# Performance work log

Hardware: AMD Instinct MI355X
Metric: run time of the kernel (lower is better)

Reference implementation:

```python
import jax, jax.numpy as jnp
import numpy as np

NUM_USER = 200000
NUM_ITEM = 100000
DIM = 64
NUM_LAYER = 2  # hardcoded in LightGCN.__init__ (lgn_single(..., num_layer=2))
AVG_DEG = 16
N = NUM_USER + NUM_ITEM
E = N * AVG_DEG
BATCH = 16384


def setup_inputs() -> dict:
    key = jax.random.key(0)
    k = jax.random.split(key, 8)
    emb_user = jax.random.normal(k[0], (NUM_USER, DIM), jnp.float32) * 0.05
    emb_item = jax.random.normal(k[1], (NUM_ITEM, DIM), jnp.float32) * 0.05
    # COO sparse normalized adjacency: out[row] += vals * x[col]
    graph_row = jax.random.randint(k[2], (E,), 0, N, dtype=jnp.int32)
    graph_col = jax.random.randint(k[3], (E,), 0, N, dtype=jnp.int32)
    graph_vals = jax.random.uniform(k[4], (E,), jnp.float32) / AVG_DEG
    user_nodes = jax.random.randint(k[5], (BATCH,), 0, NUM_USER, dtype=jnp.int32)
    pos_item_nodes = jax.random.randint(k[6], (BATCH,), 0, NUM_ITEM, dtype=jnp.int32) + NUM_USER
    neg_item_nodes = jax.random.randint(k[7], (BATCH,), 0, NUM_ITEM, dtype=jnp.int32) + NUM_USER
    return {
        "emb_user": emb_user,
        "emb_item": emb_item,
        "graph_vals": graph_vals,
        "graph_row": graph_row,
        "graph_col": graph_col,
        "user_nodes": user_nodes,
        "pos_item_nodes": pos_item_nodes,
        "neg_item_nodes": neg_item_nodes,
    }


def _spmm(vals, row, col, x):
    # torch.sparse.mm(graph, x) with graph in COO form
    return jax.ops.segment_sum(vals[:, None] * x[col], row, num_segments=N)


def reference(emb_user, emb_item, graph_vals, graph_row, graph_col,
              user_nodes, pos_item_nodes, neg_item_nodes):
    # LGN_single.forward: concat, propagate, mean over layer stack
    all_emb = jnp.concatenate([emb_user, emb_item], axis=0)  # [N, D]
    acc = all_emb
    e = all_emb
    for _ in range(NUM_LAYER):
        e = _spmm(graph_vals, graph_row, graph_col, e)
        acc = acc + e
    light_out = acc / (NUM_LAYER + 1)  # mean of stacked embeddings
    # LightGCN.forward: gather + elementwise dot scores
    u = light_out[user_nodes]          # [B, D]
    p = light_out[pos_item_nodes]      # [B, D]
    n = light_out[neg_item_nodes]      # [B, D]
    pos_scores = jnp.sum(u * p, axis=1)
    neg_scores = jnp.sum(u * n, axis=1)
    return jnp.stack([pos_scores, neg_scores])  # [2, B]
```

## Files before the change

### kernel.cpp

```cpp
#include <hip/hip_runtime.h>

#define DIM 64
#define CHUNK 8192
#define MAXNB 512
#define BSHIFT 10
#define RPB 1024
#define PADMASK 7

__device__ __forceinline__ unsigned short f2bf(float f) {
    unsigned int u = __float_as_uint(f);
    return (unsigned short)((u + 0x7FFFu + ((u >> 16) & 1u)) >> 16);
}
__device__ __forceinline__ float4 bf2f4(uint2 g) {
    float4 x;
    x.x = __uint_as_float(g.x << 16);
    x.y = __uint_as_float(g.x & 0xffff0000u);
    x.z = __uint_as_float(g.y << 16);
    x.w = __uint_as_float(g.y & 0xffff0000u);
    return x;
}

__device__ __forceinline__ int blockScan256(int v, int* sh) {
    int t = threadIdx.x;
    sh[t] = v;
    __syncthreads();
    for (int off = 1; off < 256; off <<= 1) {
        int x = (t >= off) ? sh[t - off] : 0;
        __syncthreads();
        sh[t] += x;
        __syncthreads();
    }
    return sh[t];
}


__global__ void conv2_k(const float* __restrict__ u, const float* __restrict__ it,
                        int nu, int ntot, unsigned short* __restrict__ o) {
    int i = blockIdx.x * blockDim.x + threadIdx.x;
    int stride = gridDim.x * blockDim.x;
    int n8 = ntot >> 3;
    for (int t = i; t < n8; t += stride) {
        int e = t * 8;
        const float* src = (e < nu) ? (u + e) : (it + (e - nu));
        float4 x = *(const float4*)src;
        float4 y = *(const float4*)(src + 4);
        uint4 v;
        v.x = (unsigned)f2bf(x.x) | ((unsigned)f2bf(x.y) << 16);
        v.y = (unsigned)f2bf(x.z) | ((unsigned)f2bf(x.w) << 16);
        v.z = (unsigned)f2bf(y.x) | ((unsigned)f2bf(y.y) << 16);
        v.w = (unsigned)f2bf(y.z) | ((unsigned)f2bf(y.w) << 16);
        ((uint4*)o)[t] = v;
    }
}


__global__ void p1a_hist(const int* __restrict__ row, int E, int NB,
                         int* __restrict__ counts) {
    __shared__ int h[MAXNB];
    for (int b = threadIdx.x; b < NB; b += 256) h[b] = 0;
    __syncthreads();
    int base = blockIdx.x * CHUNK;
    int end = min(base + CHUNK, E);
    int vend = base + ((end - base) & ~3);
    for (int i = base + threadIdx.x * 4; i < vend; i += 1024) {
        int4 r = *(const int4*)(row + i);
        atomicAdd(&h[r.x >> BSHIFT], 1);
        atomicAdd(&h[r.y >> BSHIFT], 1);
        atomicAdd(&h[r.z >> BSHIFT], 1);
        atomicAdd(&h[r.w >> BSHIFT], 1);
    }
    for (int i = vend + threadIdx.x; i < end; i += 256) atomicAdd(&h[row[i] >> BSHIFT], 1);
    __syncthreads();
    int blk = blockIdx.x;
    for (int b = threadIdx.x; b < NB; b += 256) counts[(size_t)blk * NB + b] = h[b];
}

__global__ void p1b_scan(int* __restrict__ counts, int NBLK, int NB,
                         int* __restrict__ bucketTotal) {
    int b = blockIdx.x, t = threadIdx.x;
    __shared__ int sh[256];
    int v[8];
    int run = 0;
#pragma unroll
    for (int i = 0; i < 8; i++) {
        int idx = t * 8 + i;
        int c = (idx < NBLK) ? counts[(size_t)idx * NB + b] : 0;
        v[i] = run;
        run += c;
    }
    int inc = blockScan256(run, sh);
    int excl = inc - run;
#pragma unroll
    for (int i = 0; i < 8; i++) {
        int idx = t * 8 + i;
        if (idx < NBLK) counts[(size_t)idx * NB + b] = v[i] + excl;
    }
    if (t == 255) bucketTotal[b] = sh[255];
}

__global__ void p_scan_tot(const int* __restrict__ bucketTotal, int NB,
                           int* __restrict__ bucketStart) {
    int t = threadIdx.x;
    __shared__ int sh[256];
    int v[8];
    int run = 0;
#pragma unroll
    for (int i = 0; i < 8; i++) {
        int idx = t * 8 + i;
        int c = (idx < NB) ? bucketTotal[idx] : 0;
        v[i] = run;
        run += c;
    }
    int inc = blockScan256(run, sh);
    int excl = inc - run;
#pragma unroll
    for (int i = 0; i < 8; i++) {
        int idx = t * 8 + i;
        if (idx < NB) bucketStart[idx] = v[i] + excl;
    }
    if (t == 255) bucketStart[NB] = sh[255];
}

__global__ void p1c_scatter(const int* __restrict__ row, const int* __restrict__ col,
                            const float* __restrict__ vals, int E, int NB,
                            const int* __restrict__ counts, const int* __restrict__ bucketStart,
                            int2* __restrict__ bdata) {
    __shared__ int cur[MAXNB];
    int blk = blockIdx.x;
    for (int b = threadIdx.x; b < NB; b += 256)
        cur[b] = bucketStart[b] + counts[(size_t)blk * NB + b];
    __syncthreads();
    int base = blk * CHUNK;
    int end = min(base + CHUNK, E);
    int vend = base + ((end - base) & ~3);
    for (int i = base + threadIdx.x * 4; i < vend; i += 1024) {
        int4 r = *(const int4*)(row + i);
        int4 c = *(const int4*)(col + i);
        float4 v = *(const float4*)(vals + i);
        int p0 = atomicAdd(&cur[r.x >> BSHIFT], 1);
        int p1 = atomicAdd(&cur[r.y >> BSHIFT], 1);
        int p2 = atomicAdd(&cur[r.z >> BSHIFT], 1);
        int p3 = atomicAdd(&cur[r.w >> BSHIFT], 1);
        bdata[p0] = make_int2(((r.x & (RPB - 1)) << 20) | c.x, __float_as_int(v.x));
        bdata[p1] = make_int2(((r.y & (RPB - 1)) << 20) | c.y, __float_as_int(v.y));
        bdata[p2] = make_int2(((r.z & (RPB - 1)) << 20) | c.z, __float_as_int(v.z));
        bdata[p3] = make_int2(((r.w & (RPB - 1)) << 20) | c.w, __float_as_int(v.w));
    }
    for (int i = vend + threadIdx.x; i < end; i += 256) {
        int r = row[i];
        int p = atomicAdd(&cur[r >> BSHIFT], 1);
        bdata[p] = make_int2(((r & (RPB - 1)) << 20) | col[i], __float_as_int(vals[i]));
    }
}

__global__ void p2_group(const int2* __restrict__ bdata, const int* __restrict__ bucketStart,
                         int NB, int N, int padSlop,
                         int* __restrict__ rowStart, int* __restrict__ rowLen,
                         int2* __restrict__ pairs) {
    __shared__ int hist[RPB];
    __shared__ int sh[256];
    __shared__ int cur[RPB];
    int b = blockIdx.x, t = threadIdx.x;
    int s0 = bucketStart[b], s1 = bucketStart[b + 1];
    int pbase = s0 + b * padSlop;
    for (int i = t; i < RPB; i += 256) hist[i] = 0;
    __syncthreads();
    for (int i = s0 + t; i < s1; i += 256)
        atomicAdd(&hist[(bdata[i].x >> 20) & (RPB - 1)], 1);
    __syncthreads();
    int v[4];
    int run = 0;
#pragma unroll
    for (int i = 0; i < 4; i++) {
        int h = hist[t * 4 + i];
        int hp = (h + PADMASK) & ~PADMASK;
        v[i] = run;
        run += hp;
    }
    int inc = blockScan256(run, sh);
    int excl = inc - run;
#pragma unroll
    for (int i = 0; i < 4; i++) {
        int r = (b << BSHIFT) + t * 4 + i;
        int st = excl + v[i];
        if (r < N) {
            int h = hist[t * 4 + i];
            rowStart[r] = pbase + st;
            rowLen[r] = (h + PADMASK) & ~PADMASK;
        }
        cur[t * 4 + i] = st;
    }
    __syncthreads();
    for (int i = s0 + t; i < s1; i += 256) {
        int2 e = bdata[i];
        int rl = (e.x >> 20) & (RPB - 1);
        int pos = atomicAdd(&cur[rl], 1);
        pairs[pbase + pos] = make_int2((e.x & 0xFFFFF) << 7, e.y);
    }
    __syncthreads();
#pragma unroll
    for (int i = 0; i < 4; i++) {
        int h = hist[t * 4 + i];
        int hp = (h + PADMASK) & ~PADMASK;
        int st = excl + v[i];
        for (int p = st + h; p < st + hp; p++)
            pairs[pbase + p] = make_int2(0, 0);
    }
}


__global__ void spmm1_k(const unsigned short* __restrict__ emb16,
                        const int* __restrict__ rowStart, const int* __restrict__ rowLen,
                        const int2* __restrict__ pairs,
                        int n_total, unsigned short* __restrict__ e1) {
    int wave = (blockIdx.x * blockDim.x + threadIdx.x) >> 6;
    int lane = threadIdx.x & 63;
    if (wave >= n_total) return;
    int eg = lane >> 4, dp = lane & 15;
    unsigned off0 = dp * 8u;
    const char* base = (const char*)emb16;
    int len = rowLen[wave];
    const int2* pp = pairs + rowStart[wave];
    float4 a0 = {0.f, 0.f, 0.f, 0.f}, a1 = {0.f, 0.f, 0.f, 0.f};
    float4 a2 = {0.f, 0.f, 0.f, 0.f}, a3 = {0.f, 0.f, 0.f, 0.f};
    int k = 0;
    for (; k + 16 <= len; k += 16) {
        int4 q0 = *(const int4*)(pp + k + 2 * eg);
        int4 q1 = *(const int4*)(pp + k + 8 + 2 * eg);
        uint2 g0 = *(const uint2*)(base + ((unsigned)q0.x + off0));
        uint2 g1 = *(const uint2*)(base + ((unsigned)q0.z + off0));
        uint2 g2 = *(const uint2*)(base + ((unsigned)q1.x + off0));
        uint2 g3 = *(const uint2*)(base + ((unsigned)q1.z + off0));
        float v0 = __int_as_float(q0.y), v1 = __int_as_float(q0.w);
        float v2 = __int_as_float(q1.y), v3 = __int_as_float(q1.w);
        float4 x0 = bf2f4(g0), x1 = bf2f4(g1), x2 = bf2f4(g2), x3 = bf2f4(g3);
        a0.x += v0 * x0.x; a0.y += v0 * x0.y; a0.z += v0 * x0.z; a0.w += v0 * x0.w;
        a1.x += v1 * x1.x; a1.y += v1 * x1.y; a1.z += v1 * x1.z; a1.w += v1 * x1.w;
        a2.x += v2 * x2.x; a2.y += v2 * x2.y; a2.z += v2 * x2.z; a2.w += v2 * x2.w;
        a3.x += v3 * x3.x; a3.y += v3 * x3.y; a3.z += v3 * x3.z; a3.w += v3 * x3.w;
    }
    for (; k < len; k += 8) {
        int4 q0 = *(const int4*)(pp + k + 2 * eg);
        uint2 g0 = *(const uint2*)(base + ((unsigned)q0.x + off0));
        uint2 g1 = *(const uint2*)(base + ((unsigned)q0.z + off0));
        float v0 = __int_as_float(q0.y), v1 = __int_as_float(q0.w);
        float4 x0 = bf2f4(g0), x1 = bf2f4(g1);
        a0.x += v0 * x0.x; a0.y += v0 * x0.y; a0.z += v0 * x0.z; a0.w += v0 * x0.w;
        a1.x += v1 * x1.x; a1.y += v1 * x1.y; a1.z += v1 * x1.z; a1.w += v1 * x1.w;
    }
    float4 s;
    s.x = (a0.x + a1.x) + (a2.x + a3.x);
    s.y = (a0.y + a1.y) + (a2.y + a3.y);
    s.z = (a0.z + a1.z) + (a2.z + a3.z);
    s.w = (a0.w + a1.w) + (a2.w + a3.w);
    s.x += __shfl_xor(s.x, 16); s.y += __shfl_xor(s.y, 16);
    s.z += __shfl_xor(s.z, 16); s.w += __shfl_xor(s.w, 16);
    s.x += __shfl_xor(s.x, 32); s.y += __shfl_xor(s.y, 32);
    s.z += __shfl_xor(s.z, 32); s.w += __shfl_xor(s.w, 32);
    if (eg == 0) {
        uint2 o;
        o.x = (unsigned)f2bf(s.x) | ((unsigned)f2bf(s.y) << 16);
        o.y = (unsigned)f2bf(s.z) | ((unsigned)f2bf(s.w) << 16);
        *(uint2*)(e1 + (size_t)wave * DIM + dp * 4) = o;
    }
}


__global__ void final_k(const float* __restrict__ emb_user, const float* __restrict__ emb_item,
                        int n_user, const unsigned short* __restrict__ e1,
                        const int* __restrict__ rowStart, const int* __restrict__ rowLen,
                        const int2* __restrict__ pairs,
                        const int* __restrict__ u_nodes, const int* __restrict__ p_nodes,
                        const int* __restrict__ n_nodes, int B, float* __restrict__ out) {
    int wave = (blockIdx.x * blockDim.x + threadIdx.x) >> 6;
    int lane = threadIdx.x & 63;
    if (wave >= B) return;
    int eg = lane >> 4, dp = lane & 15;
    unsigned off0 = dp * 8u;
    const char* base = (const char*)e1;
    int nid[3] = {u_nodes[wave], p_nodes[wave], n_nodes[wave]};
    float4 l[3];
#pragma unroll
    for (int j = 0; j < 3; j++) {
        int r = nid[j];
        const float* base0 = (r < n_user) ? (emb_user + (size_t)r * DIM)
                                          : (emb_item + (size_t)(r - n_user) * DIM);
        float4 acc = *(const float4*)(base0 + dp * 4);
        float4 t1 = bf2f4(*(const uint2*)(e1 + (size_t)r * DIM + dp * 4));
        acc.x += t1.x; acc.y += t1.y; acc.z += t1.z; acc.w += t1.w;
        int len = rowLen[r];
        const int2* pp = pairs + rowStart[r];
        float4 a0 = {0.f, 0.f, 0.f, 0.f}, a1 = {0.f, 0.f, 0.f, 0.f};
        float4 a2 = {0.f, 0.f, 0.f, 0.f}, a3 = {0.f, 0.f, 0.f, 0.f};
        int k = 0;
        for (; k + 16 <= len; k += 16) {
            int4 q0 = *(const int4*)(pp + k + 2 * eg);
            int4 q1 = *(const int4*)(pp + k + 8 + 2 * eg);
            uint2 g0 = *(const uint2*)(base + ((unsigned)q0.x + off0));
            uint2 g1 = *(const uint2*)(base + ((unsigned)q0.z + off0));
            uint2 g2 = *(const uint2*)(base + ((unsigned)q1.x + off0));
            uint2 g3 = *(const uint2*)(base + ((unsigned)q1.z + off0));
            float v0 = __int_as_float(q0.y), v1 = __int_as_float(q0.w);
            float v2 = __int_as_float(q1.y), v3 = __int_as_float(q1.w);
            float4 x0 = bf2f4(g0), x1 = bf2f4(g1), x2 = bf2f4(g2), x3 = bf2f4(g3);
            a0.x += v0 * x0.x; a0.y += v0 * x0.y; a0.z += v0 * x0.z; a0.w += v0 * x0.w;
            a1.x += v1 * x1.x; a1.y += v1 * x1.y; a1.z += v1 * x1.z; a1.w += v1 * x1.w;
            a2.x += v2 * x2.x; a2.y += v2 * x2.y; a2.z += v2 * x2.z; a2.w += v2 * x2.w;
            a3.x += v3 * x3.x; a3.y += v3 * x3.y; a3.z += v3 * x3.z; a3.w += v3 * x3.w;
        }
        for (; k < len; k += 8) {
            int4 q0 = *(const int4*)(pp + k + 2 * eg);
            uint2 g0 = *(const uint2*)(base + ((unsigned)q0.x + off0));
            uint2 g1 = *(const uint2*)(base + ((unsigned)q0.z + off0));
            float v0 = __int_as_float(q0.y), v1 = __int_as_float(q0.w);
            float4 x0 = bf2f4(g0), x1 = bf2f4(g1);
            a0.x += v0 * x0.x; a0.y += v0 * x0.y; a0.z += v0 * x0.z; a0.w += v0 * x0.w;
            a1.x += v1 * x1.x; a1.y += v1 * x1.y; a1.z += v1 * x1.z; a1.w += v1 * x1.w;
        }
        float4 s;
        s.x = (a0.x + a1.x) + (a2.x + a3.x);
        s.y = (a0.y + a1.y) + (a2.y + a3.y);
        s.z = (a0.z + a1.z) + (a2.z + a3.z);
        s.w = (a0.w + a1.w) + (a2.w + a3.w);
        s.x += __shfl_xor(s.x, 16); s.y += __shfl_xor(s.y, 16);
        s.z += __shfl_xor(s.z, 16); s.w += __shfl_xor(s.w, 16);
        s.x += __shfl_xor(s.x, 32); s.y += __shfl_xor(s.y, 32);
        s.z += __shfl_xor(s.z, 32); s.w += __shfl_xor(s.w, 32);
        l[j].x = (acc.x + s.x) * (1.0f / 3.0f);
        l[j].y = (acc.y + s.y) * (1.0f / 3.0f);
        l[j].z = (acc.z + s.z) * (1.0f / 3.0f);
        l[j].w = (acc.w + s.w) * (1.0f / 3.0f);
    }
    float ps = l[0].x * l[1].x + l[0].y * l[1].y + l[0].z * l[1].z + l[0].w * l[1].w;
    float ns = l[0].x * l[2].x + l[0].y * l[2].y + l[0].z * l[2].z + l[0].w * l[2].w;
    ps += __shfl_xor(ps, 1); ns += __shfl_xor(ns, 1);
    ps += __shfl_xor(ps, 2); ns += __shfl_xor(ns, 2);
    ps += __shfl_xor(ps, 4); ns += __shfl_xor(ns, 4);
    ps += __shfl_xor(ps, 8); ns += __shfl_xor(ns, 8);
    if (lane == 0) {
        out[wave] = ps;
        out[B + wave] = ns;
    }
}

extern "C" void kernel_launch(void* const* d_in, const int* in_sizes, int n_in,
                              void* d_out, int out_size, void* d_ws, size_t ws_size,
                              hipStream_t stream) {
    const float* emb_user = (const float*)d_in[0];
    const float* emb_item = (const float*)d_in[1];
    const float* gvals    = (const float*)d_in[2];
    const int*   grow     = (const int*)d_in[3];
    const int*   gcol     = (const int*)d_in[4];
    const int*   unodes   = (const int*)d_in[5];
    const int*   pnodes   = (const int*)d_in[6];
    const int*   nnodes   = (const int*)d_in[7];
    float* out = (float*)d_out;

    int n_user = in_sizes[0] / DIM;
    int n_item = in_sizes[1] / DIM;
    int N = n_user + n_item;
    int E = in_sizes[2];
    int B = in_sizes[5];
    int NB = (N + RPB - 1) >> BSHIFT;
    int NBLK = (E + CHUNK - 1) / CHUNK;
    int padSlop = RPB * PADMASK;

    char* ws = (char*)d_ws;
    size_t off = 0;
    auto alloc = [&](size_t bytes) -> void* {
        void* p = ws + off;
        off = (off + bytes + 255) & ~(size_t)255;
        return p;
    };
    size_t embBytes = (size_t)N * DIM * 2;
    size_t countsBytes = (size_t)NBLK * NB * 4;
    size_t regionBBytes = (size_t)E * 8 > embBytes ? (size_t)E * 8 : embBytes;
    size_t regionABytes = countsBytes > embBytes ? countsBytes : embBytes;
    size_t pairsBytes = ((size_t)E + (size_t)NB * padSlop) * 8;

    int*  rowStart    = (int*)alloc((size_t)N * 4);
    int*  rowLen      = (int*)alloc((size_t)N * 4);
    int*  bucketTotal = (int*)alloc((size_t)MAXNB * 4);
    int*  bucketStart = (int*)alloc((size_t)(MAXNB + 1) * 4);
    int2* pairs       = (int2*)alloc(pairsBytes);
    char* regionB = (char*)alloc(regionBBytes);
    int2*           bdata = (int2*)regionB;
    unsigned short* emb16 = (unsigned short*)regionB;
    char* regionA = (char*)alloc(regionABytes);
    int*            counts = (int*)regionA;
    unsigned short* e1     = (unsigned short*)regionA;
    (void)n_in; (void)out_size; (void)ws_size;

    p1a_hist<<<NBLK, 256, 0, stream>>>(grow, E, NB, counts);
    p1b_scan<<<NB, 256, 0, stream>>>(counts, NBLK, NB, bucketTotal);
    p_scan_tot<<<1, 256, 0, stream>>>(bucketTotal, NB, bucketStart);
    p1c_scatter<<<NBLK, 256, 0, stream>>>(grow, gcol, gvals, E, NB, counts, bucketStart, bdata);
    p2_group<<<NB, 256, 0, stream>>>(bdata, bucketStart, NB, N, padSlop,
                                     rowStart, rowLen, pairs);

    conv2_k<<<2048, 256, 0, stream>>>(emb_user, emb_item, n_user * DIM, N * DIM, emb16);

    spmm1_k<<<(N + 3) / 4, 256, 0, stream>>>(emb16, rowStart, rowLen, pairs, N, e1);
    final_k<<<(B + 3) / 4, 256, 0, stream>>>(emb_user, emb_item, n_user, e1,
                                             rowStart, rowLen, pairs,
                                             unodes, pnodes, nnodes, B, out);
}
```

Before: 307.4 us.

## Fuse bf16 embedding conversion into histogram kernel and use nontemporal streaming loads

When the workspace is large enough, the bf16 embedding buffer gets its own region instead of aliasing the COO bucket buffer. The float-to-bf16 conversion can then run as extra blocks inside the histogram kernel rather than as a separate launch after grouping. Streaming reads of row/col/vals, bdata, rowStart/rowLen and the pairs array become nontemporal loads, so they are less likely to evict the embedding rows that are gathered from cache. The cost is extra workspace and a runtime branch on workspace size, with the old aliasing path kept as a fallback.

```diff
diff --git a/kernel.cpp b/kernel.cpp
--- a/kernel.cpp
+++ b/kernel.cpp
@@ -6,6 +6,12 @@
 #define BSHIFT 10
 #define RPB 1024
 #define PADMASK 7
+#define CONVB 1024
+
+typedef int   iv2 __attribute__((ext_vector_type(2)));
+typedef int   iv4 __attribute__((ext_vector_type(4)));
+typedef float fv4 __attribute__((ext_vector_type(4)));
+#define NTL(p) __builtin_nontemporal_load(p)
 
 __device__ __forceinline__ unsigned short f2bf(float f) {
     unsigned int u = __float_as_uint(f);
@@ -34,45 +40,45 @@
 }
 
 
-__global__ void conv2_k(const float* __restrict__ u, const float* __restrict__ it,
-                        int nu, int ntot, unsigned short* __restrict__ o) {
-    int i = blockIdx.x * blockDim.x + threadIdx.x;
-    int stride = gridDim.x * blockDim.x;
-    int n8 = ntot >> 3;
-    for (int t = i; t < n8; t += stride) {
-        int e = t * 8;
-        const float* src = (e < nu) ? (u + e) : (it + (e - nu));
-        float4 x = *(const float4*)src;
-        float4 y = *(const float4*)(src + 4);
-        uint4 v;
-        v.x = (unsigned)f2bf(x.x) | ((unsigned)f2bf(x.y) << 16);
-        v.y = (unsigned)f2bf(x.z) | ((unsigned)f2bf(x.w) << 16);
-        v.z = (unsigned)f2bf(y.x) | ((unsigned)f2bf(y.y) << 16);
-        v.w = (unsigned)f2bf(y.z) | ((unsigned)f2bf(y.w) << 16);
-        ((uint4*)o)[t] = v;
-    }
-}
-
-
-__global__ void p1a_hist(const int* __restrict__ row, int E, int NB,
-                         int* __restrict__ counts) {
+__global__ void p1a_conv(const int* __restrict__ row, int E, int NB,
+                         int* __restrict__ counts,
+                         const float* __restrict__ u, const float* __restrict__ it,
+                         int nu, int ntot, unsigned short* __restrict__ o, int NBLK) {
     __shared__ int h[MAXNB];
-    for (int b = threadIdx.x; b < NB; b += 256) h[b] = 0;
-    __syncthreads();
-    int base = blockIdx.x * CHUNK;
-    int end = min(base + CHUNK, E);
-    int vend = base + ((end - base) & ~3);
-    for (int i = base + threadIdx.x * 4; i < vend; i += 1024) {
-        int4 r = *(const int4*)(row + i);
-        atomicAdd(&h[r.x >> BSHIFT], 1);
-        atomicAdd(&h[r.y >> BSHIFT], 1);
-        atomicAdd(&h[r.z >> BSHIFT], 1);
-        atomicAdd(&h[r.w >> BSHIFT], 1);
-    }
-    for (int i = vend + threadIdx.x; i < end; i += 256) atomicAdd(&h[row[i] >> BSHIFT], 1);
-    __syncthreads();
     int blk = blockIdx.x;
-    for (int b = threadIdx.x; b < NB; b += 256) counts[(size_t)blk * NB + b] = h[b];
+    if (blk < NBLK) {
+        for (int b = threadIdx.x; b < NB; b += 256) h[b] = 0;
+        __syncthreads();
+        int base = blk * CHUNK;
+        int end = min(base + CHUNK, E);
+        int vend = base + ((end - base) & ~3);
+        for (int i = base + threadIdx.x * 4; i < vend; i += 1024) {
+            iv4 r = NTL((const iv4*)(row + i));
+            atomicAdd(&h[r.x >> BSHIFT], 1);
+            atomicAdd(&h[r.y >> BSHIFT], 1);
+            atomicAdd(&h[r.z >> BSHIFT], 1);
+            atomicAdd(&h[r.w >> BSHIFT], 1);
+        }
+        for (int i = vend + threadIdx.x; i < end; i += 256) atomicAdd(&h[row[i] >> BSHIFT], 1);
+        __syncthreads();
+        for (int b = threadIdx.x; b < NB; b += 256) counts[(size_t)blk * NB + b] = h[b];
+    } else {
+        int i = (blk - NBLK) * 256 + threadIdx.x;
+        int stride = CONVB * 256;
+        int n8 = ntot >> 3;
+        for (int t = i; t < n8; t += stride) {
+            int e = t * 8;
+            const float* src = (e < nu) ? (u + e) : (it + (e - nu));
+            fv4 x = NTL((const fv4*)src);
+            fv4 y = NTL((const fv4*)(src + 4));
+            uint4 v;
+            v.x = (unsigned)f2bf(x.x) | ((unsigned)f2bf(x.y) << 16);
+            v.y = (unsigned)f2bf(x.z) | ((unsigned)f2bf(x.w) << 16);
+            v.z = (unsigned)f2bf(y.x) | ((unsigned)f2bf(y.y) << 16);
+            v.w = (unsigned)f2bf(y.z) | ((unsigned)f2bf(y.w) << 16);
+            ((uint4*)o)[t] = v;
+        }
+    }
 }
 
 __global__ void p1b_scan(int* __restrict__ counts, int NBLK, int NB,
@@ -134,9 +140,9 @@
     int end = min(base + CHUNK, E);
     int vend = base + ((end - base) & ~3);
     for (int i = base + threadIdx.x * 4; i < vend; i += 1024) {
-        int4 r = *(const int4*)(row + i);
-        int4 c = *(const int4*)(col + i);
-        float4 v = *(const float4*)(vals + i);
+        iv4 r = NTL((const iv4*)(row + i));
+        iv4 c = NTL((const iv4*)(col + i));
+        fv4 v = NTL((const fv4*)(vals + i));
         int p0 = atomicAdd(&cur[r.x >> BSHIFT], 1);
         int p1 = atomicAdd(&cur[r.y >> BSHIFT], 1);
         int p2 = atomicAdd(&cur[r.z >> BSHIFT], 1);
@@ -192,7 +198,7 @@
     }
     __syncthreads();
     for (int i = s0 + t; i < s1; i += 256) {
-        int2 e = bdata[i];
+        iv2 e = NTL((const iv2*)(bdata + i));
         int rl = (e.x >> 20) & (RPB - 1);
         int pos = atomicAdd(&cur[rl], 1);
         pairs[pbase + pos] = make_int2((e.x & 0xFFFFF) << 7, e.y);
@@ -219,14 +225,14 @@
     int eg = lane >> 4, dp = lane & 15;
     unsigned off0 = dp * 8u;
     const char* base = (const char*)emb16;
-    int len = rowLen[wave];
-    const int2* pp = pairs + rowStart[wave];
+    int len = NTL(rowLen + wave);
+    const int2* pp = pairs + NTL(rowStart + wave);
     float4 a0 = {0.f, 0.f, 0.f, 0.f}, a1 = {0.f, 0.f, 0.f, 0.f};
     float4 a2 = {0.f, 0.f, 0.f, 0.f}, a3 = {0.f, 0.f, 0.f, 0.f};
     int k = 0;
     for (; k + 16 <= len; k += 16) {
-        int4 q0 = *(const int4*)(pp + k + 2 * eg);
-        int4 q1 = *(const int4*)(pp + k + 8 + 2 * eg);
+        iv4 q0 = NTL((const iv4*)(pp + k + 2 * eg));
+        iv4 q1 = NTL((const iv4*)(pp + k + 8 + 2 * eg));
         uint2 g0 = *(const uint2*)(base + ((unsigned)q0.x + off0));
         uint2 g1 = *(const uint2*)(base + ((unsigned)q0.z + off0));
         uint2 g2 = *(const uint2*)(base + ((unsigned)q1.x + off0));
@@ -240,7 +246,7 @@
         a3.x += v3 * x3.x; a3.y += v3 * x3.y; a3.z += v3 * x3.z; a3.w += v3 * x3.w;
     }
     for (; k < len; k += 8) {
-        int4 q0 = *(const int4*)(pp + k + 2 * eg);
+        iv4 q0 = NTL((const iv4*)(pp + k + 2 * eg));
         uint2 g0 = *(const uint2*)(base + ((unsigned)q0.x + off0));
         uint2 g1 = *(const uint2*)(base + ((unsigned)q0.z + off0));
         float v0 = __int_as_float(q0.y), v1 = __int_as_float(q0.w);
@@ -294,8 +300,8 @@
         float4 a2 = {0.f, 0.f, 0.f, 0.f}, a3 = {0.f, 0.f, 0.f, 0.f};
         int k = 0;
         for (; k + 16 <= len; k += 16) {
-            int4 q0 = *(const int4*)(pp + k + 2 * eg);
-            int4 q1 = *(const int4*)(pp + k + 8 + 2 * eg);
+            iv4 q0 = NTL((const iv4*)(pp + k + 2 * eg));
+            iv4 q1 = NTL((const iv4*)(pp + k + 8 + 2 * eg));
             uint2 g0 = *(const uint2*)(base + ((unsigned)q0.x + off0));
             uint2 g1 = *(const uint2*)(base + ((unsigned)q0.z + off0));
             uint2 g2 = *(const uint2*)(base + ((unsigned)q1.x + off0));
@@ -309,7 +315,7 @@
             a3.x += v3 * x3.x; a3.y += v3 * x3.y; a3.z += v3 * x3.z; a3.w += v3 * x3.w;
         }
         for (; k < len; k += 8) {
-            int4 q0 = *(const int4*)(pp + k + 2 * eg);
+            iv4 q0 = NTL((const iv4*)(pp + k + 2 * eg));
             uint2 g0 = *(const uint2*)(base + ((unsigned)q0.x + off0));
             uint2 g1 = *(const uint2*)(base + ((unsigned)q0.z + off0));
             float v0 = __int_as_float(q0.y), v1 = __int_as_float(q0.w);
@@ -343,6 +349,25 @@
     }
 }
 
+__global__ void conv2_k(const float* __restrict__ u, const float* __restrict__ it,
+                        int nu, int ntot, unsigned short* __restrict__ o) {
+    int i = blockIdx.x * blockDim.x + threadIdx.x;
+    int stride = gridDim.x * blockDim.x;
+    int n8 = ntot >> 3;
+    for (int t = i; t < n8; t += stride) {
+        int e = t * 8;
+        const float* src = (e < nu) ? (u + e) : (it + (e - nu));
+        fv4 x = NTL((const fv4*)src);
+        fv4 y = NTL((const fv4*)(src + 4));
+        uint4 v;
+        v.x = (unsigned)f2bf(x.x) | ((unsigned)f2bf(x.y) << 16);
+        v.y = (unsigned)f2bf(x.z) | ((unsigned)f2bf(x.w) << 16);
+        v.z = (unsigned)f2bf(y.x) | ((unsigned)f2bf(y.y) << 16);
+        v.w = (unsigned)f2bf(y.z) | ((unsigned)f2bf(y.w) << 16);
+        ((uint4*)o)[t] = v;
+    }
+}
+
 extern "C" void kernel_launch(void* const* d_in, const int* in_sizes, int n_in,
                               void* d_out, int out_size, void* d_ws, size_t ws_size,
                               hipStream_t stream) {
@@ -365,6 +390,17 @@
     int NBLK = (E + CHUNK - 1) / CHUNK;
     int padSlop = RPB * PADMASK;
 
+    auto align256 = [](size_t x) { return (x + 255) & ~(size_t)255; };
+    size_t embBytes = (size_t)N * DIM * 2;
+    size_t countsBytes = (size_t)NBLK * NB * 4;
+    size_t bdataBytes = (size_t)E * 8;
+    size_t regionABytes = countsBytes > embBytes ? countsBytes : embBytes;
+    size_t pairsBytes = ((size_t)E + (size_t)NB * padSlop) * 8;
+    size_t fixedBytes = align256((size_t)N * 4) * 2 + align256((size_t)MAXNB * 4) +
+                        align256((size_t)(MAXNB + 1) * 4) + align256(pairsBytes) +
+                        align256(regionABytes);
+    bool sepEmb = fixedBytes + align256(bdataBytes) + align256(embBytes) <= ws_size;
+
     char* ws = (char*)d_ws;
     size_t off = 0;
     auto alloc = [&](size_t bytes) -> void* {
@@ -372,33 +408,37 @@
         off = (off + bytes + 255) & ~(size_t)255;
         return p;
     };
-    size_t embBytes = (size_t)N * DIM * 2;
-    size_t countsBytes = (size_t)NBLK * NB * 4;
-    size_t regionBBytes = (size_t)E * 8 > embBytes ? (size_t)E * 8 : embBytes;
-    size_t regionABytes = countsBytes > embBytes ? countsBytes : embBytes;
-    size_t pairsBytes = ((size_t)E + (size_t)NB * padSlop) * 8;
-
     int*  rowStart    = (int*)alloc((size_t)N * 4);
     int*  rowLen      = (int*)alloc((size_t)N * 4);
     int*  bucketTotal = (int*)alloc((size_t)MAXNB * 4);
     int*  bucketStart = (int*)alloc((size_t)(MAXNB + 1) * 4);
     int2* pairs       = (int2*)alloc(pairsBytes);
-    char* regionB = (char*)alloc(regionBBytes);
-    int2*           bdata = (int2*)regionB;
-    unsigned short* emb16 = (unsigned short*)regionB;
+    int2* bdata;
+    unsigned short* emb16;
+    if (sepEmb) {
+        bdata = (int2*)alloc(bdataBytes);
+        emb16 = (unsigned short*)alloc(embBytes);
+    } else {
+        char* regionB = (char*)alloc(bdataBytes > embBytes ? bdataBytes : embBytes);
+        bdata = (int2*)regionB;
+        emb16 = (unsigned short*)regionB;
+    }
     char* regionA = (char*)alloc(regionABytes);
     int*            counts = (int*)regionA;
     unsigned short* e1     = (unsigned short*)regionA;
-    (void)n_in; (void)out_size; (void)ws_size;
-
-    p1a_hist<<<NBLK, 256, 0, stream>>>(grow, E, NB, counts);
+    (void)n_in; (void)out_size;
+
+    int nConv = sepEmb ? CONVB : 0;
+    p1a_conv<<<NBLK + nConv, 256, 0, stream>>>(grow, E, NB, counts,
+                                               emb_user, emb_item, n_user * DIM, N * DIM,
+                                               emb16, NBLK);
     p1b_scan<<<NB, 256, 0, stream>>>(counts, NBLK, NB, bucketTotal);
     p_scan_tot<<<1, 256, 0, stream>>>(bucketTotal, NB, bucketStart);
     p1c_scatter<<<NBLK, 256, 0, stream>>>(grow, gcol, gvals, E, NB, counts, bucketStart, bdata);
     p2_group<<<NB, 256, 0, stream>>>(bdata, bucketStart, NB, N, padSlop,
                                      rowStart, rowLen, pairs);
-
-    conv2_k<<<2048, 256, 0, stream>>>(emb_user, emb_item, n_user * DIM, N * DIM, emb16);
+    if (!sepEmb)
+        conv2_k<<<2048, 256, 0, stream>>>(emb_user, emb_item, n_user * DIM, N * DIM, emb16);
 
     spmm1_k<<<(N + 3) / 4, 256, 0, stream>>>(emb16, rowStart, rowLen, pairs, N, e1);
     final_k<<<(B + 3) / 4, 256, 0, stream>>>(emb_user, emb_item, n_user, e1,
```

Result: slower. 343.6 us (+11.8%).
